# Kernel optimization log

Hardware: AMD Instinct MI355X
Metric: run time of the kernel (lower is better)

The kernel has to match this reference:

```python
import jax, jax.numpy as jnp
import numpy as np

B, P, Q, D_IN, H, DR = 16, 4096, 512, 512, 256, 256


def setup_inputs() -> dict:
    key = jax.random.key(0)
    ks = jax.random.split(key, 6)
    passage = jax.random.normal(ks[0], (B, P, D_IN), dtype=jnp.float32)
    question = jax.random.normal(ks[1], (B, Q, D_IN), dtype=jnp.float32)
    rep = jax.random.normal(ks[2], (B, Q, DR), dtype=jnp.float32)
    rep_p = jax.random.normal(ks[3], (B, P, DR), dtype=jnp.float32)
    p_mask = jnp.zeros((B, P), dtype=bool)  # True = padding position
    q_mask = jnp.zeros((B, Q), dtype=bool)
    # xavier-uniform-like init for U weight, stored as [in, out]
    limit = float(np.sqrt(6.0 / (D_IN + H)))
    W = jax.random.uniform(ks[4], (D_IN, H), dtype=jnp.float32, minval=-limit, maxval=limit)
    D = jnp.ones((1, H), dtype=jnp.float32)
    return {"passage": passage, "p_mask": p_mask, "question": question,
            "q_mask": q_mask, "rep": rep, "rep_p": rep_p, "W": W, "D": D,
            "is_training": 0}


def reference(passage, p_mask, question, q_mask, rep, rep_p, W, D, is_training):
    # inference path (is_training falsy): no dropout
    Up = jax.nn.relu(passage @ W)              # [B, P, H]
    Uq = jax.nn.relu(question @ W) * D         # [B, Q, H], scaled by diagonal D
    scores = jnp.einsum('bph,bqh->bpq', Up, Uq)  # [B, P, Q]
    # question -> passage direction (rep_p is not None)
    scores_T = jnp.where(p_mask[:, None, :], -jnp.inf, scores.transpose(0, 2, 1))  # [B, Q, P]
    alpha_p = jax.nn.softmax(scores_T, axis=-1)
    output_q = jnp.einsum('bqp,bpd->bqd', alpha_p, rep_p)  # [B, Q, DR]
    # passage -> question direction
    scores_m = jnp.where(q_mask[:, None, :], -jnp.inf, scores)  # [B, P, Q]
    alpha = jax.nn.softmax(scores_m, axis=-1)
    output = jnp.einsum('bpq,bqd->bpd', alpha, rep)  # [B, P, DR]
    return (output, output_q)
```

## Files before the change

### kernel.cpp

```cpp
#include <hip/hip_runtime.h>


typedef float  f32x4   __attribute__((ext_vector_type(4)));
typedef float  float4v __attribute__((ext_vector_type(4)));
typedef short  short8v __attribute__((ext_vector_type(8)));
typedef unsigned short us4 __attribute__((ext_vector_type(4)));
typedef unsigned short us8v __attribute__((ext_vector_type(8)));

#define MFMA16(a,b,c) __builtin_amdgcn_mfma_f32_16x16x32_bf16((a),(b),(c),0,0,0)

__device__ __forceinline__ unsigned short f2bf(float f) {
  unsigned int u = __builtin_bit_cast(unsigned int, f);
  u += 0x7FFFu + ((u >> 16) & 1u);
  return (unsigned short)(u >> 16);
}
__device__ __forceinline__ float bf2f(unsigned short h) {
  unsigned int u = (unsigned int)h << 16;
  return __builtin_bit_cast(float, u);
}
__device__ __forceinline__ void split2(float v, unsigned short& h, unsigned short& l) {
  h = f2bf(v);
  l = f2bf(v - bf2f(h));
}
__device__ __forceinline__ unsigned short enc16(float a, float cm) {
  float x = (a - cm + 20.f) * 3276.8f + 0.5f;
  x = fminf(fmaxf(x, 0.f), 65535.f);
  return (unsigned short)x;
}

__device__ __forceinline__ void transpose_body(
    const float* __restrict__ src, unsigned short* __restrict__ dst,
    unsigned short* __restrict__ dstl, int srows, size_t r0, size_t c0,
    int t, float* smemf)
{
#pragma unroll
  for (int j = 0; j < 4; ++j) {
    int idx = j * 256 + t;
    int r = idx >> 4, c4 = (idx & 15) * 4;
    float4v v = *(const float4v*)&src[(r0 + (size_t)r) * 256 + c0 + c4];
    smemf[r * 65 + c4 + 0] = v[0]; smemf[r * 65 + c4 + 1] = v[1];
    smemf[r * 65 + c4 + 2] = v[2]; smemf[r * 65 + c4 + 3] = v[3];
  }
  __syncthreads();
#pragma unroll
  for (int j = 0; j < 4; ++j) {
    int idx = j * 256 + t;
    int dr = idx >> 4, p4 = (idx & 15) * 4;
    size_t o = (c0 + (size_t)dr) * (size_t)srows + r0 + p4;
    if (!dstl) {
      us4 oh;
#pragma unroll
      for (int e = 0; e < 4; ++e) oh[e] = f2bf(smemf[(p4 + e) * 65 + dr]);
      *(us4*)&dst[o] = oh;
    } else {
      us4 oh, ol;
#pragma unroll
      for (int e = 0; e < 4; ++e) {
        unsigned short h, l; split2(smemf[(p4 + e) * 65 + dr], h, l);
        oh[e] = h; ol[e] = l;
      }
      *(us4*)&dst[o] = oh;
      *(us4*)&dstl[o] = ol;
    }
  }
}

template<int APPLY_D>
__device__ __forceinline__ void ugemm_body(
    const float* __restrict__ X,
    const unsigned short* __restrict__ Wth, const unsigned short* __restrict__ Wtl,
    const float* __restrict__ Dv,
    unsigned short* __restrict__ Uh, unsigned short* __restrict__ Ul,
    size_t m0, int t, unsigned char* smem)
{
  unsigned short* lAh = (unsigned short*)smem;
  unsigned short* lAl = (unsigned short*)(smem + 5120);
  unsigned short* lBh = (unsigned short*)(smem + 10240);
  unsigned short* lBl = (unsigned short*)(smem + 30720);
  const int w = t >> 6, l = t & 63;
  const int l15 = l & 15, lg = l >> 4, kr = lg * 8;
  const int arow = t >> 2, ac = (t & 3) * 8;
  const float* asrc = X + (m0 + arow) * 512 + ac;

  f32x4 acc[4][4] = {};
  float4v va0, va1;
  short8v vbh[4], vbl[4];

  va0 = *(const float4v*)(asrc);
  va1 = *(const float4v*)(asrc + 4);
#pragma unroll
  for (int j = 0; j < 4; ++j) {
    int idx = j * 256 + t;
    int row = idx >> 2, c = (idx & 3) * 8;
    size_t g = (size_t)row * 512 + c;
    vbh[j] = *(const short8v*)&Wth[g];
    vbl[j] = *(const short8v*)&Wtl[g];
  }

  for (int k0 = 0; k0 < 512; k0 += 32) {
    short8v ph, pl;
#pragma unroll
    for (int e = 0; e < 4; ++e) {
      unsigned short h, lo;
      split2(va0[e], h, lo); ph[e] = (short)h; pl[e] = (short)lo;
      split2(va1[e], h, lo); ph[4 + e] = (short)h; pl[4 + e] = (short)lo;
    }
    __syncthreads();
    *(short8v*)&lAh[arow * 40 + ac] = ph;
    *(short8v*)&lAl[arow * 40 + ac] = pl;
#pragma unroll
    for (int j = 0; j < 4; ++j) {
      int idx = j * 256 + t;
      int row = idx >> 2, c = (idx & 3) * 8;
      *(short8v*)&lBh[row * 40 + c] = vbh[j];
      *(short8v*)&lBl[row * 40 + c] = vbl[j];
    }
    __syncthreads();
    if (k0 < 480) {
      va0 = *(const float4v*)(asrc + k0 + 32);
      va1 = *(const float4v*)(asrc + k0 + 36);
#pragma unroll
      for (int j = 0; j < 4; ++j) {
        int idx = j * 256 + t;
        int row = idx >> 2, c = (idx & 3) * 8;
        size_t g = (size_t)row * 512 + k0 + 32 + c;
        vbh[j] = *(const short8v*)&Wth[g];
        vbl[j] = *(const short8v*)&Wtl[g];
      }
    }
    short8v ah[4], al[4];
#pragma unroll
    for (int mi = 0; mi < 4; ++mi) {
      ah[mi] = *(const short8v*)&lAh[(mi * 16 + l15) * 40 + kr];
      al[mi] = *(const short8v*)&lAl[(mi * 16 + l15) * 40 + kr];
    }
#pragma unroll
    for (int ni = 0; ni < 4; ++ni) {
      int rr = (w * 64 + ni * 16 + l15) * 40 + kr;
      short8v bh = *(const short8v*)&lBh[rr];
      short8v bl = *(const short8v*)&lBl[rr];
#pragma unroll
      for (int mi = 0; mi < 4; ++mi) {
        acc[mi][ni] = MFMA16(ah[mi], bh, acc[mi][ni]);
        acc[mi][ni] = MFMA16(ah[mi], bl, acc[mi][ni]);
        acc[mi][ni] = MFMA16(al[mi], bh, acc[mi][ni]);
      }
    }
  }
#pragma unroll
  for (int mi = 0; mi < 4; ++mi)
#pragma unroll
    for (int ni = 0; ni < 4; ++ni)
#pragma unroll
      for (int r = 0; r < 4; ++r) {
        size_t row = m0 + mi * 16 + lg * 4 + r;
        int col = w * 64 + ni * 16 + l15;
        float v = acc[mi][ni][r];
        v = v > 0.f ? v : 0.f;
        if (APPLY_D) v *= Dv[col];
        unsigned short h, lo; split2(v, h, lo);
        Uh[row * 256 + col] = h;
        Ul[row * 256 + col] = lo;
      }
}

__global__ __launch_bounds__(256) void transpose_w(
    const float* __restrict__ W,
    unsigned short* __restrict__ Wth, unsigned short* __restrict__ Wtl)
{
  __shared__ float lTf[64 * 65];
  const int blk = blockIdx.x;
  transpose_body(W, Wth, Wtl, 512, (size_t)(blk >> 2) * 64,
                 (size_t)(blk & 3) * 64, threadIdx.x, lTf);
}

__global__ __launch_bounds__(256) void prep_mega(
    const float* __restrict__ passage, const float* __restrict__ question,
    const float* __restrict__ rep, const float* __restrict__ rep_p,
    const unsigned short* __restrict__ Wth, const unsigned short* __restrict__ Wtl,
    const float* __restrict__ Dv,
    unsigned short* __restrict__ Uph, unsigned short* __restrict__ Upl,
    unsigned short* __restrict__ Uqh, unsigned short* __restrict__ Uql,
    unsigned short* __restrict__ repT, unsigned short* __restrict__ repTp)
{
  __shared__ __align__(16) unsigned char smem[51200];
  const int blk = blockIdx.x;
  const int t = threadIdx.x;
  if (blk < 1024) {
    ugemm_body<0>(passage, Wth, Wtl, nullptr, Uph, Upl,
                  (size_t)blk * 64, t, smem);
  } else if (blk < 1152) {
    ugemm_body<1>(question, Wth, Wtl, Dv, Uqh, Uql,
                  (size_t)(blk - 1024) * 64, t, smem);
  } else if (blk < 5248) {
    int rel = blk - 1152;
    int b = rel >> 8, tb = rel & 255;
    transpose_body(rep_p + (size_t)b * 4096 * 256,
                   repTp + (size_t)b * 256 * 4096, nullptr, 4096,
                   (size_t)(tb >> 2) * 64, (size_t)(tb & 3) * 64, t,
                   (float*)smem);
  } else {
    int rel = blk - 5248;
    int b = rel >> 5, tb = rel & 31;
    transpose_body(rep + (size_t)b * 512 * 256,
                   repT + (size_t)b * 256 * 512, nullptr, 512,
                   (size_t)(tb >> 2) * 64, (size_t)(tb & 3) * 64, t,
                   (float*)smem);
  }
}

__global__ __launch_bounds__(256) void transpose_all(
    const float* __restrict__ W, const float* __restrict__ rep,
    const float* __restrict__ rep_p,
    unsigned short* __restrict__ Wth, unsigned short* __restrict__ Wtl,
    unsigned short* __restrict__ repT, unsigned short* __restrict__ repTp)
{
  __shared__ float lTf[64 * 65];
  const int blk = blockIdx.x;
  const int t = threadIdx.x;
  if (blk < 4096) {
    int b = blk >> 8, tb = blk & 255;
    transpose_body(rep_p + (size_t)b * 4096 * 256,
                   repTp + (size_t)b * 256 * 4096, nullptr, 4096,
                   (size_t)(tb >> 2) * 64, (size_t)(tb & 3) * 64, t, lTf);
  } else if (blk < 4608) {
    int rel = blk - 4096; int b = rel >> 5, tb = rel & 31;
    transpose_body(rep + (size_t)b * 512 * 256,
                   repT + (size_t)b * 256 * 512, nullptr, 512,
                   (size_t)(tb >> 2) * 64, (size_t)(tb & 3) * 64, t, lTf);
  } else {
    int rel = blk - 4608;
    transpose_body(W, Wth, Wtl, 512, (size_t)(rel >> 2) * 64,
                   (size_t)(rel & 3) * 64, t, lTf);
  }
}

template<int APPLY_D>
__global__ __launch_bounds__(256) void ugemm_kernel(
    const float* __restrict__ X,
    const unsigned short* __restrict__ Wth, const unsigned short* __restrict__ Wtl,
    const float* __restrict__ Dv,
    unsigned short* __restrict__ Uh, unsigned short* __restrict__ Ul)
{
  __shared__ __align__(16) unsigned char smem[51200];
  ugemm_body<APPLY_D>(X, Wth, Wtl, Dv, Uh, Ul,
                      (size_t)blockIdx.x * 64, threadIdx.x, smem);
}

template<int STORE_S>
__global__ __launch_bounds__(512, 4) void dir2_kernel(
    const unsigned short* __restrict__ Uph, const unsigned short* __restrict__ Upl,
    const unsigned short* __restrict__ Uqh, const unsigned short* __restrict__ Uql,
    const unsigned short* __restrict__ repT, const unsigned char* __restrict__ qmask,
    const unsigned char* __restrict__ pmask, unsigned short* __restrict__ St,
    float* __restrict__ colmaxP, float* __restrict__ out)
{
  __shared__ __align__(16) unsigned char smem[68608];
  unsigned short* probs = (unsigned short*)smem;
  float* smax = (float*)(smem + 66560);
  float* ssum = (float*)(smem + 67584);

  const int id = blockIdx.x;
  const int b  = (id & 7) | ((id >> 9) << 3);
  const int p0 = ((id >> 3) & 63) * 64;
  const int t = threadIdx.x;
  const int w = t >> 6, l = t & 63;
  const int wr = w >> 2, wc = w & 3;
  const int l15 = l & 15, lg = l >> 4, kr = lg * 8;
  const int srow = t >> 2, sc = (t & 3) * 8;

  const unsigned short* UqBh = Uqh + (size_t)b * 512 * 256;
  const unsigned short* UqBl = Uql + (size_t)b * 512 * 256;
  const size_t aoff = ((size_t)b * 4096 + p0 + wr * 32 + l15) * 256 + kr;
  const unsigned short* pAh0 = Uph + aoff;
  const unsigned short* pAh1 = pAh0 + 16 * 256;
  const unsigned short* pAl0 = Upl + aoff;
  const unsigned short* pAl1 = pAl0 + 16 * 256;

  auto lbh = [&](int buf) { return (unsigned short*)(smem + buf * 20480); };
  auto lbl = [&](int buf) { return (unsigned short*)(smem + buf * 20480 + 10240); };

  f32x4 acc[2][8] = {};
  short8v cah0, cah1, cal0, cal1;
  short8v nah0, nah1, nal0, nal1;
  short8v rh, rl;

  cah0 = *(const short8v*)&pAh0[0];
  cah1 = *(const short8v*)&pAh1[0];
  cal0 = *(const short8v*)&pAl0[0];
  cal1 = *(const short8v*)&pAl1[0];
  {
    size_t g = (size_t)srow * 256 + sc;
    rh = *(const short8v*)&UqBh[g];
    rl = *(const short8v*)&UqBl[g];
  }
  *(short8v*)&lbh(0)[srow * 40 + sc] = rh;
  *(short8v*)&lbl(0)[srow * 40 + sc] = rl;
  __syncthreads();

  for (int k0 = 0; k0 < 8; ++k0) {
#pragma unroll
    for (int qh = 0; qh < 4; ++qh) {
      const int cur = qh & 1;
      const bool last = (k0 == 7) && (qh == 3);
      if (!last) {
        int nk0 = (qh == 3) ? k0 + 1 : k0;
        int nqh = (qh == 3) ? 0 : qh + 1;
        size_t g = (size_t)(nqh * 128 + srow) * 256 + nk0 * 32 + sc;
        rh = *(const short8v*)&UqBh[g];
        rl = *(const short8v*)&UqBl[g];
      }
      if (qh == 3 && k0 < 7) {
        size_t ao = (size_t)(k0 + 1) * 32;
        nah0 = *(const short8v*)&pAh0[ao];
        nah1 = *(const short8v*)&pAh1[ao];
        nal0 = *(const short8v*)&pAl0[ao];
        nal1 = *(const short8v*)&pAl1[ao];
      }
      const unsigned short* bhp = lbh(cur);
      const unsigned short* blp = lbl(cur);
#pragma unroll
      for (int qi = 0; qi < 2; ++qi) {
        int rr = (wc * 32 + qi * 16 + l15) * 40 + kr;
        short8v bh = *(const short8v*)&bhp[rr];
        short8v bl = *(const short8v*)&blp[rr];
        int j = qh * 2 + qi;
        acc[0][j] = MFMA16(cah0, bh, acc[0][j]);
        acc[0][j] = MFMA16(cah0, bl, acc[0][j]);
        acc[0][j] = MFMA16(cal0, bh, acc[0][j]);
        acc[1][j] = MFMA16(cah1, bh, acc[1][j]);
        acc[1][j] = MFMA16(cah1, bl, acc[1][j]);
        acc[1][j] = MFMA16(cal1, bh, acc[1][j]);
      }
      if (!last) {
        *(short8v*)&lbh(cur ^ 1)[srow * 40 + sc] = rh;
        *(short8v*)&lbl(cur ^ 1)[srow * 40 + sc] = rl;
      }
      if (qh == 3 && k0 < 7) { cah0 = nah0; cah1 = nah1; cal0 = nal0; cal1 = nal1; }
      __syncthreads();
    }
  }
  if (STORE_S) {
    const unsigned char* pmk = pmask + (size_t)b * 4096 + p0 + wr * 32;
    unsigned int pmw0 = *(const unsigned int*)&pmk[lg * 4];
    unsigned int pmw1 = *(const unsigned int*)&pmk[16 + lg * 4];
#pragma unroll
    for (int j = 0; j < 8; ++j) {
      int qcol = ((j >> 1) << 7) + wc * 32 + ((j & 1) << 4) + l15;
      float a0[4], a1[4];
      float cm = -1e30f;
#pragma unroll
      for (int r = 0; r < 4; ++r) {
        a0[r] = ((pmw0 >> (8 * r)) & 0xFFu) ? -1e30f : acc[0][j][r];
        a1[r] = ((pmw1 >> (8 * r)) & 0xFFu) ? -1e30f : acc[1][j][r];
        cm = fmaxf(cm, fmaxf(a0[r], a1[r]));
      }
      cm = fmaxf(cm, __shfl_xor(cm, 16));
      cm = fmaxf(cm, __shfl_xor(cm, 32));
      us4 e0, e1;
#pragma unroll
      for (int r = 0; r < 4; ++r) {
        e0[r] = enc16(a0[r], cm);
        e1[r] = enc16(a1[r], cm);
      }
      size_t sb = ((size_t)b * 512 + qcol) * 4096 + p0 + wr * 32 + lg * 4;
      *(us4*)&St[sb]      = e0;
      *(us4*)&St[sb + 16] = e1;
      if (l < 16)
        colmaxP[((size_t)b * 128 + (p0 >> 5) + wr) * 512 + qcol] = cm;
    }
  }
  const unsigned char* qm = qmask + (size_t)b * 512;
#pragma unroll
  for (int j = 0; j < 8; ++j) {
    int qcol = ((j >> 1) << 7) + wc * 32 + ((j & 1) << 4) + l15;
    if (qm[qcol]) {
#pragma unroll
      for (int mi = 0; mi < 2; ++mi)
#pragma unroll
        for (int r = 0; r < 4; ++r) acc[mi][j][r] = -1e30f;
    }
  }
#pragma unroll
  for (int mi = 0; mi < 2; ++mi)
#pragma unroll
    for (int r = 0; r < 4; ++r) {
      float v = acc[mi][0][r];
#pragma unroll
      for (int j = 1; j < 8; ++j) v = fmaxf(v, acc[mi][j][r]);
      v = fmaxf(v, __shfl_xor(v, 1)); v = fmaxf(v, __shfl_xor(v, 2));
      v = fmaxf(v, __shfl_xor(v, 4)); v = fmaxf(v, __shfl_xor(v, 8));
      if (l15 == 0) smax[wc * 64 + wr * 32 + mi * 16 + lg * 4 + r] = v;
    }
  __syncthreads();
  float Mx[2][4];
#pragma unroll
  for (int mi = 0; mi < 2; ++mi)
#pragma unroll
    for (int r = 0; r < 4; ++r) {
      int row = wr * 32 + mi * 16 + lg * 4 + r;
      Mx[mi][r] = fmaxf(fmaxf(smax[row], smax[64 + row]),
                        fmaxf(smax[128 + row], smax[192 + row]));
    }
  float rs[2][4] = {};
#pragma unroll
  for (int mi = 0; mi < 2; ++mi)
#pragma unroll
    for (int j = 0; j < 8; ++j)
#pragma unroll
      for (int r = 0; r < 4; ++r) {
        float ev = __expf(acc[mi][j][r] - Mx[mi][r]);
        acc[mi][j][r] = ev;
        rs[mi][r] += ev;
      }
#pragma unroll
  for (int mi = 0; mi < 2; ++mi)
#pragma unroll
    for (int r = 0; r < 4; ++r) {
      float v = rs[mi][r];
      v += __shfl_xor(v, 1); v += __shfl_xor(v, 2);
      v += __shfl_xor(v, 4); v += __shfl_xor(v, 8);
      if (l15 == 0) ssum[wc * 64 + wr * 32 + mi * 16 + lg * 4 + r] = v;
    }
#pragma unroll
  for (int mi = 0; mi < 2; ++mi)
#pragma unroll
    for (int j = 0; j < 8; ++j) {
      int qcol = ((j >> 1) << 7) + wc * 32 + ((j & 1) << 4) + l15;
#pragma unroll
      for (int r = 0; r < 4; ++r)
        probs[(wr * 32 + mi * 16 + lg * 4 + r) * 520 + qcol] = f2bf(acc[mi][j][r]);
    }
  __syncthreads();
  const unsigned short* rT = repT + (size_t)b * 131072;
  float invv[4][4];
#pragma unroll
  for (int mi = 0; mi < 4; ++mi)
#pragma unroll
    for (int r = 0; r < 4; ++r) {
      int row = mi * 16 + lg * 4 + r;
      invv[mi][r] = 1.0f / (ssum[row] + ssum[64 + row] +
                            ssum[128 + row] + ssum[192 + row]);
    }
  f32x4 acc2[4][2] = {};
  const unsigned short* rTb = rT + (size_t)(w * 32 + l15) * 512 + kr;
  short8v cb0 = *(const short8v*)(rTb);
  short8v cb1 = *(const short8v*)(rTb + 16 * 512);
  for (int k0 = 0; k0 < 512; k0 += 32) {
    int kn = (k0 + 32) & 511;
    short8v nb0 = *(const short8v*)(rTb + kn);
    short8v nb1 = *(const short8v*)(rTb + 16 * 512 + kn);
    short8v a0 = *(const short8v*)&probs[(l15) * 520 + k0 + kr];
    short8v a1 = *(const short8v*)&probs[(16 + l15) * 520 + k0 + kr];
    short8v a2 = *(const short8v*)&probs[(32 + l15) * 520 + k0 + kr];
    short8v a3 = *(const short8v*)&probs[(48 + l15) * 520 + k0 + kr];
    acc2[0][0] = MFMA16(a0, cb0, acc2[0][0]);
    acc2[1][0] = MFMA16(a1, cb0, acc2[1][0]);
    acc2[2][0] = MFMA16(a2, cb0, acc2[2][0]);
    acc2[3][0] = MFMA16(a3, cb0, acc2[3][0]);
    acc2[0][1] = MFMA16(a0, cb1, acc2[0][1]);
    acc2[1][1] = MFMA16(a1, cb1, acc2[1][1]);
    acc2[2][1] = MFMA16(a2, cb1, acc2[2][1]);
    acc2[3][1] = MFMA16(a3, cb1, acc2[3][1]);
    cb0 = nb0; cb1 = nb1;
  }
#pragma unroll
  for (int mi = 0; mi < 4; ++mi)
#pragma unroll
    for (int di = 0; di < 2; ++di)
#pragma unroll
      for (int r = 0; r < 4; ++r) {
        int row = p0 + mi * 16 + lg * 4 + r;
        int col = w * 32 + di * 16 + l15;
        out[((size_t)b * 4096 + row) * 256 + col] = acc2[mi][di][r] * invv[mi][r];
      }
}

__global__ __launch_bounds__(256) void dir1_pv(
    const unsigned short* __restrict__ St, const float* __restrict__ colmaxP,
    const unsigned short* __restrict__ repTp,
    float* __restrict__ accP, float* __restrict__ mlP)
{
  __shared__ unsigned short lAe[2][32 * 72];
  const int id = blockIdx.x;
  const int xcd = id & 7, r0 = id >> 3;
  const int b = xcd * 2 + (r0 >> 6);
  const int rem = r0 & 63;
  const int qt = rem >> 2, ch = rem & 3;
  const int q0 = qt * 32, pbeg = ch * 1024;
  const int pi = (b * 16 + qt) * 4 + ch;
  const int NT = 16;

  const int t = threadIdx.x;
  const int w = t >> 6, l = t & 63;
  const int l15 = l & 15, lg = l >> 4, kr = lg * 8;
  const int srow = t >> 3, sp = (t & 7) * 8;

  const float* cmq = colmaxP + (size_t)b * 128 * 512 + q0 + srow;
  float mq_s;
  {
    const int part = t & 7;
    float m = -1e30f;
#pragma unroll
    for (int j = 0; j < 16; ++j)
      m = fmaxf(m, cmq[(size_t)(part + j * 8) * 512]);
    m = fmaxf(m, __shfl_xor(m, 1));
    m = fmaxf(m, __shfl_xor(m, 2));
    m = fmaxf(m, __shfl_xor(m, 4));
    mq_s = m;
  }
  const unsigned short* Sb = St + ((size_t)b * 512 + q0 + srow) * 4096;
  const unsigned short* vtb = repTp + ((size_t)b * 256 + w * 64 + l15) * 4096;
  float rsum = 0.f;
  f32x4 acc[2][4] = {};
  us8v u; float cmv;
  short8v bvA[2][4], bvB[2][4];

  auto STAGE_LOAD = [&](int tile) {
    int pelem = pbeg + tile * 64 + sp;
    u = *(const us8v*)(Sb + pelem);
    cmv = cmq[(size_t)(pelem >> 5) * 512];
  };
  auto STAGE_FINISH = [&](int buf) {
    float base = cmv - 20.f - mq_s;
    short8v pk;
#pragma unroll
    for (int e = 0; e < 8; ++e) {
      float ev = __expf((float)u[e] * (1.f / 3276.8f) + base);
      rsum += ev;
      pk[e] = (short)f2bf(ev);
    }
    *(short8v*)&lAe[buf][srow * 72 + sp] = pk;
  };
  auto BV_LOAD = [&](int tile, short8v (&bv)[2][4]) {
    int p0v = pbeg + tile * 64;
#pragma unroll
    for (int ks = 0; ks < 2; ++ks)
#pragma unroll
      for (int di = 0; di < 4; ++di)
        bv[ks][di] = *(const short8v*)&vtb[(size_t)(di * 16) * 4096 + p0v + ks * 32 + kr];
  };
  auto COMPUTE = [&](int buf, short8v (&bv)[2][4]) {
#pragma unroll
    for (int ks = 0; ks < 2; ++ks) {
      short8v pa0 = *(const short8v*)&lAe[buf][l15 * 72 + ks * 32 + kr];
      short8v pa1 = *(const short8v*)&lAe[buf][(16 + l15) * 72 + ks * 32 + kr];
#pragma unroll
      for (int di = 0; di < 4; ++di) {
        acc[0][di] = MFMA16(pa0, bv[ks][di], acc[0][di]);
        acc[1][di] = MFMA16(pa1, bv[ks][di], acc[1][di]);
      }
    }
  };

  STAGE_LOAD(0);
  BV_LOAD(0, bvA);
  STAGE_FINISH(0);
  STAGE_LOAD(1);
  __syncthreads();

#pragma unroll 1
  for (int tt = 0; tt < NT; tt += 2) {
    const bool has1 = (tt + 1 < NT), has2 = (tt + 2 < NT), has3 = (tt + 3 < NT);
    if (has1) BV_LOAD(tt + 1, bvB);
    COMPUTE(0, bvA);
    if (has1) STAGE_FINISH(1);
    if (has2) STAGE_LOAD(tt + 2);
    __syncthreads();
    if (has1) {
      if (has2) BV_LOAD(tt + 2, bvA);
      COMPUTE(1, bvB);
      if (has2) STAGE_FINISH(0);
      if (has3) STAGE_LOAD(tt + 3);
      __syncthreads();
    }
  }

  rsum += __shfl_xor(rsum, 1);
  rsum += __shfl_xor(rsum, 2);
  rsum += __shfl_xor(rsum, 4);
  if ((t & 7) == 0) mlP[(size_t)pi * 32 + srow] = rsum;

  float* ab = accP + (size_t)pi * 32 * 256;
#pragma unroll
  for (int mi = 0; mi < 2; ++mi)
#pragma unroll
    for (int di = 0; di < 4; ++di)
#pragma unroll
      for (int r = 0; r < 4; ++r) {
        int row = mi * 16 + lg * 4 + r;
        int col = w * 64 + di * 16 + l15;
        ab[(size_t)row * 256 + col] = acc[mi][di][r];
      }
}

__global__ __launch_bounds__(256) void merge4_kernel(
    const float* __restrict__ accP, const float* __restrict__ mlP,
    float* __restrict__ outq)
{
  const int g = blockIdx.x * 256 + threadIdx.x;
  const int row = g >> 6;
  const int d0 = (g & 63) * 4;
  const int b = row >> 9, q = row & 511;
  const int qt = q >> 5, ri = q & 31;
  const int pbase = (b * 16 + qt) * 4;
  float s = 0.f;
  float4v o = {0.f, 0.f, 0.f, 0.f};
#pragma unroll
  for (int c = 0; c < 4; ++c) {
    s += mlP[(size_t)(pbase + c) * 32 + ri];
    float4v a = *(const float4v*)&accP[((size_t)(pbase + c) * 32 + ri) * 256 + d0];
#pragma unroll
    for (int k = 0; k < 4; ++k) o[k] += a[k];
  }
  float inv = 1.0f / s;
#pragma unroll
  for (int k = 0; k < 4; ++k) o[k] *= inv;
  *(float4v*)&outq[(size_t)row * 256 + d0] = o;
}

__global__ __launch_bounds__(256) void dir1_partial(
    const unsigned short* __restrict__ Uph, const unsigned short* __restrict__ Upl,
    const unsigned short* __restrict__ Uqh, const unsigned short* __restrict__ Uql,
    const unsigned short* __restrict__ repTp, const unsigned char* __restrict__ pmask,
    float* __restrict__ accP, float* __restrict__ mlP)
{
  __shared__ __align__(16) unsigned char smem[39424];
  unsigned short* lAh = (unsigned short*)smem;
  unsigned short* lAl = (unsigned short*)(smem + 16896);
  unsigned short* lP  = (unsigned short*)(smem + 33792);
  float* smax = (float*)(smem + 38400);
  float* ssum = (float*)(smem + 38912);

  const int id  = blockIdx.x;
  const int xcd = id & 7, rr0 = id >> 3;
  const int b   = xcd * 2 + (rr0 >> 6);
  const int rem = rr0 & 63;
  const int qt  = rem >> 2, ch = rem & 3;
  const int q0  = qt * 32;
  const int pbeg = ch * 1024;
  const int pi  = (b * 16 + qt) * 4 + ch;

  const int t = threadIdx.x;
  const int w = t >> 6, l = t & 63;
  const int l15 = l & 15, lg = l >> 4, kr = lg * 8;

#pragma unroll
  for (int j = 0; j < 4; ++j) {
    int idx = j * 256 + t;
    int row = idx >> 5, c = (idx & 31) * 8;
    size_t g = ((size_t)b * 512 + q0 + row) * 256 + c;
    *(short8v*)&lAh[row * 264 + c] = *(const short8v*)&Uqh[g];
    *(short8v*)&lAl[row * 264 + c] = *(const short8v*)&Uql[g];
  }
  float m_r[2][4], l_r[2][4];
#pragma unroll
  for (int mi = 0; mi < 2; ++mi)
#pragma unroll
    for (int r = 0; r < 4; ++r) { m_r[mi][r] = -1e30f; l_r[mi][r] = 0.f; }
  f32x4 accO[2][4] = {};
  const size_t upoff = ((size_t)b * 4096 + w * 16 + l15) * 256;
  const unsigned short* upbh = Uph + upoff;
  const unsigned short* upbl = Upl + upoff;
  const unsigned short* vtb = repTp + (size_t)b * 1048576;
  const unsigned char* pm = pmask + (size_t)b * 4096;
  __syncthreads();

  for (int p0 = pbeg; p0 < pbeg + 1024; p0 += 64) {
    f32x4 s[2] = {};
#pragma unroll
    for (int k0 = 0; k0 < 256; k0 += 32) {
      short8v ah0 = *(const short8v*)&lAh[l15 * 264 + k0 + kr];
      short8v ah1 = *(const short8v*)&lAh[(16 + l15) * 264 + k0 + kr];
      short8v al0 = *(const short8v*)&lAl[l15 * 264 + k0 + kr];
      short8v al1 = *(const short8v*)&lAl[(16 + l15) * 264 + k0 + kr];
      short8v bvh = *(const short8v*)&upbh[(size_t)p0 * 256 + k0 + kr];
      short8v bvl = *(const short8v*)&upbl[(size_t)p0 * 256 + k0 + kr];
      s[0] = MFMA16(ah0, bvh, s[0]);
      s[0] = MFMA16(ah0, bvl, s[0]);
      s[0] = MFMA16(al0, bvh, s[0]);
      s[1] = MFMA16(ah1, bvh, s[1]);
      s[1] = MFMA16(ah1, bvl, s[1]);
      s[1] = MFMA16(al1, bvh, s[1]);
    }
    if (pm[p0 + w * 16 + l15]) {
#pragma unroll
      for (int mi = 0; mi < 2; ++mi)
#pragma unroll
        for (int r = 0; r < 4; ++r) s[mi][r] = -1e30f;
    }
#pragma unroll
    for (int mi = 0; mi < 2; ++mi)
#pragma unroll
      for (int r = 0; r < 4; ++r) {
        float v = s[mi][r];
        v = fmaxf(v, __shfl_xor(v, 1)); v = fmaxf(v, __shfl_xor(v, 2));
        v = fmaxf(v, __shfl_xor(v, 4)); v = fmaxf(v, __shfl_xor(v, 8));
        if (l15 == 0) smax[w * 32 + mi * 16 + lg * 4 + r] = v;
      }
    __syncthreads();
    float mnew[2][4], fsc[2][4], e[2][4];
#pragma unroll
    for (int mi = 0; mi < 2; ++mi)
#pragma unroll
      for (int r = 0; r < 4; ++r) {
        int row = mi * 16 + lg * 4 + r;
        float tm = fmaxf(fmaxf(smax[row], smax[32 + row]),
                         fmaxf(smax[64 + row], smax[96 + row]));
        float mn = fmaxf(m_r[mi][r], tm);
        mnew[mi][r] = mn;
        fsc[mi][r] = __expf(m_r[mi][r] - mn);
        e[mi][r] = __expf(s[mi][r] - mn);
      }
#pragma unroll
    for (int mi = 0; mi < 2; ++mi)
#pragma unroll
      for (int r = 0; r < 4; ++r) {
        float v = e[mi][r];
        v += __shfl_xor(v, 1); v += __shfl_xor(v, 2);
        v += __shfl_xor(v, 4); v += __shfl_xor(v, 8);
        if (l15 == 0) ssum[w * 32 + mi * 16 + lg * 4 + r] = v;
        lP[(mi * 16 + lg * 4 + r) * 72 + w * 16 + l15] = f2bf(e[mi][r]);
      }
    __syncthreads();
#pragma unroll
    for (int mi = 0; mi < 2; ++mi)
#pragma unroll
      for (int r = 0; r < 4; ++r) {
        int row = mi * 16 + lg * 4 + r;
        float ts = ssum[row] + ssum[32 + row] + ssum[64 + row] + ssum[96 + row];
        l_r[mi][r] = l_r[mi][r] * fsc[mi][r] + ts;
        m_r[mi][r] = mnew[mi][r];
      }
#pragma unroll
    for (int mi = 0; mi < 2; ++mi)
#pragma unroll
      for (int di = 0; di < 4; ++di)
#pragma unroll
        for (int r = 0; r < 4; ++r) accO[mi][di][r] *= fsc[mi][r];
#pragma unroll
    for (int ks = 0; ks < 64; ks += 32) {
      short8v pa0 = *(const short8v*)&lP[l15 * 72 + ks + kr];
      short8v pa1 = *(const short8v*)&lP[(16 + l15) * 72 + ks + kr];
#pragma unroll
      for (int di = 0; di < 4; ++di) {
        short8v bv = *(const short8v*)&vtb[(size_t)(w * 64 + di * 16 + l15) * 4096 + p0 + ks + kr];
        accO[0][di] = MFMA16(pa0, bv, accO[0][di]);
        accO[1][di] = MFMA16(pa1, bv, accO[1][di]);
      }
    }
  }
  float* ab = accP + (size_t)pi * 32 * 256;
#pragma unroll
  for (int mi = 0; mi < 2; ++mi)
#pragma unroll
    for (int di = 0; di < 4; ++di)
#pragma unroll
      for (int r = 0; r < 4; ++r) {
        int row = mi * 16 + lg * 4 + r;
        int col = w * 64 + di * 16 + l15;
        ab[(size_t)row * 256 + col] = accO[mi][di][r];
      }
  if (w == 0 && l15 == 0) {
#pragma unroll
    for (int mi = 0; mi < 2; ++mi)
#pragma unroll
      for (int r = 0; r < 4; ++r) {
        int row = mi * 16 + lg * 4 + r;
        mlP[((size_t)pi * 32 + row) * 2 + 0] = m_r[mi][r];
        mlP[((size_t)pi * 32 + row) * 2 + 1] = l_r[mi][r];
      }
  }
}

__global__ __launch_bounds__(256) void merge_kernel(
    const float* __restrict__ accP, const float* __restrict__ mlP,
    float* __restrict__ outq)
{
  const int g = blockIdx.x * 256 + threadIdx.x;
  const int row = g >> 6;
  const int d0 = (g & 63) * 4;
  const int b = row >> 9, q = row & 511;
  const int qt = q >> 5, ri = q & 31;
  const int pbase = (b * 16 + qt) * 4;
  float m[4], lv[4];
  float M = -1e30f;
#pragma unroll
  for (int c = 0; c < 4; ++c) {
    m[c]  = mlP[((size_t)(pbase + c) * 32 + ri) * 2 + 0];
    lv[c] = mlP[((size_t)(pbase + c) * 32 + ri) * 2 + 1];
    M = fmaxf(M, m[c]);
  }
  float s = 0.f;
  float4v o = {0.f, 0.f, 0.f, 0.f};
#pragma unroll
  for (int c = 0; c < 4; ++c) {
    float e = __expf(m[c] - M);
    s += e * lv[c];
    float4v a = *(const float4v*)&accP[((size_t)(pbase + c) * 32 + ri) * 256 + d0];
#pragma unroll
    for (int k = 0; k < 4; ++k) o[k] += e * a[k];
  }
  float inv = 1.0f / s;
#pragma unroll
  for (int k = 0; k < 4; ++k) o[k] *= inv;
  *(float4v*)&outq[(size_t)row * 256 + d0] = o;
}

extern "C" void kernel_launch(void* const* d_in, const int* in_sizes, int n_in,
                              void* d_out, int out_size, void* d_ws, size_t ws_size,
                              hipStream_t stream) {
  (void)in_sizes; (void)n_in; (void)out_size;
  const float* passage        = (const float*)d_in[0];
  const unsigned char* p_mask = (const unsigned char*)d_in[1];
  const float* question       = (const float*)d_in[2];
  const unsigned char* q_mask = (const unsigned char*)d_in[3];
  const float* rep            = (const float*)d_in[4];
  const float* rep_p          = (const float*)d_in[5];
  const float* W              = (const float*)d_in[6];
  const float* Dv             = (const float*)d_in[7];

  unsigned short* Wth   = (unsigned short*)d_ws;
  unsigned short* Wtl   = Wth   + 131072;
  unsigned short* repT  = Wtl   + 131072;
  unsigned short* repTp = repT  + 2097152;
  unsigned short* Uqh   = repTp + 16777216;
  unsigned short* Uql   = Uqh   + 2097152;
  unsigned short* Uph   = Uql   + 2097152;
  unsigned short* Upl   = Uph   + 16777216;
  unsigned short* StU = (unsigned short*)((char*)d_ws + 113770496ULL);
  float* colmaxP      = (float*)((char*)d_ws + 180879360ULL);
  const size_t NEEDED = 185073664ULL;

  float* out  = (float*)d_out;
  float* outq = out + (size_t)16 * 4096 * 256;

  if (ws_size >= NEEDED) {
    float* accP4 = (float*)Uph;
    float* mlP4  = (float*)Uqh;
    transpose_w<<<32, 256, 0, stream>>>(W, Wth, Wtl);
    prep_mega<<<5760, 256, 0, stream>>>(passage, question, rep, rep_p,
                                        Wth, Wtl, Dv, Uph, Upl, Uqh, Uql,
                                        repT, repTp);
    dir2_kernel<1><<<1024, 512, 0, stream>>>(Uph, Upl, Uqh, Uql, repT,
                                             q_mask, p_mask, StU, colmaxP, out);
    dir1_pv<<<1024, 256, 0, stream>>>(StU, colmaxP, repTp, accP4, mlP4);
    merge4_kernel<<<2048, 256, 0, stream>>>(accP4, mlP4, outq);
  } else {
    float* accP = out;
    float* mlP  = (float*)Wth;
    transpose_all<<<4640, 256, 0, stream>>>(W, rep, rep_p, Wth, Wtl, repT, repTp);
    ugemm_kernel<0><<<1024, 256, 0, stream>>>(passage,  Wth, Wtl, nullptr, Uph, Upl);
    ugemm_kernel<1><<<128,  256, 0, stream>>>(question, Wth, Wtl, Dv,      Uqh, Uql);
    dir1_partial<<<1024, 256, 0, stream>>>(Uph, Upl, Uqh, Uql, repTp, p_mask, accP, mlP);
    merge_kernel<<<2048, 256, 0, stream>>>(accP, mlP, outq);
    dir2_kernel<0><<<1024, 512, 0, stream>>>(Uph, Upl, Uqh, Uql, repT,
                                             q_mask, nullptr, nullptr, nullptr, out);
  }
}
```

Baseline: 312.2 us.

## Double dir2 P-tile to 128 rows with 1024-thread blocks and split PV stage

Each dir2 block now covers 128 passage rows with 16 waves instead of 64 rows with 8 waves. The staged Uq tiles in shared memory are therefore reused across twice as many rows, and only half the threads load them. Because the probability buffer still holds 64 rows, the softmax-times-rep stage runs in two halves, with each wave producing 16 output columns. The cost is that repT is re-read per half, there are fewer MFMAs per B load, and the block count halves. The register cap from launch bounds of 1024 threads with 4 blocks may also cause spills.

```diff
diff --git a/kernel.cpp b/kernel.cpp
--- a/kernel.cpp
+++ b/kernel.cpp
@@ -248,26 +248,27 @@
 }
 
 template<int STORE_S>
-__global__ __launch_bounds__(512, 4) void dir2_kernel(
+__global__ __launch_bounds__(1024, 4) void dir2_kernel(
     const unsigned short* __restrict__ Uph, const unsigned short* __restrict__ Upl,
     const unsigned short* __restrict__ Uqh, const unsigned short* __restrict__ Uql,
     const unsigned short* __restrict__ repT, const unsigned char* __restrict__ qmask,
     const unsigned char* __restrict__ pmask, unsigned short* __restrict__ St,
     float* __restrict__ colmaxP, float* __restrict__ out)
 {
-  __shared__ __align__(16) unsigned char smem[68608];
+  __shared__ __align__(16) unsigned char smem[70656];
   unsigned short* probs = (unsigned short*)smem;
   float* smax = (float*)(smem + 66560);
-  float* ssum = (float*)(smem + 67584);
+  float* ssum = (float*)(smem + 68608);
 
   const int id = blockIdx.x;
-  const int b  = (id & 7) | ((id >> 9) << 3);
-  const int p0 = ((id >> 3) & 63) * 64;
+  const int xcd = id & 7, r0b = id >> 3;
+  const int b = xcd * 2 + (r0b >> 5);
+  const int p0 = (r0b & 31) * 128;
   const int t = threadIdx.x;
   const int w = t >> 6, l = t & 63;
   const int wr = w >> 2, wc = w & 3;
   const int l15 = l & 15, lg = l >> 4, kr = lg * 8;
-  const int srow = t >> 2, sc = (t & 3) * 8;
+  const int srow = (t >> 2) & 127, sc = (t & 3) * 8;
 
   const unsigned short* UqBh = Uqh + (size_t)b * 512 * 256;
   const unsigned short* UqBl = Uql + (size_t)b * 512 * 256;
@@ -289,13 +290,13 @@
   cah1 = *(const short8v*)&pAh1[0];
   cal0 = *(const short8v*)&pAl0[0];
   cal1 = *(const short8v*)&pAl1[0];
-  {
+  if (t < 512) {
     size_t g = (size_t)srow * 256 + sc;
     rh = *(const short8v*)&UqBh[g];
     rl = *(const short8v*)&UqBl[g];
-  }
-  *(short8v*)&lbh(0)[srow * 40 + sc] = rh;
-  *(short8v*)&lbl(0)[srow * 40 + sc] = rl;
+    *(short8v*)&lbh(0)[srow * 40 + sc] = rh;
+    *(short8v*)&lbl(0)[srow * 40 + sc] = rl;
+  }
   __syncthreads();
 
   for (int k0 = 0; k0 < 8; ++k0) {
@@ -303,7 +304,7 @@
     for (int qh = 0; qh < 4; ++qh) {
       const int cur = qh & 1;
       const bool last = (k0 == 7) && (qh == 3);
-      if (!last) {
+      if (!last && t < 512) {
         int nk0 = (qh == 3) ? k0 + 1 : k0;
         int nqh = (qh == 3) ? 0 : qh + 1;
         size_t g = (size_t)(nqh * 128 + srow) * 256 + nk0 * 32 + sc;
@@ -332,7 +333,7 @@
         acc[1][j] = MFMA16(cah1, bl, acc[1][j]);
         acc[1][j] = MFMA16(cal1, bh, acc[1][j]);
       }
-      if (!last) {
+      if (!last && t < 512) {
         *(short8v*)&lbh(cur ^ 1)[srow * 40 + sc] = rh;
         *(short8v*)&lbl(cur ^ 1)[srow * 40 + sc] = rl;
       }
@@ -390,7 +391,7 @@
       for (int j = 1; j < 8; ++j) v = fmaxf(v, acc[mi][j][r]);
       v = fmaxf(v, __shfl_xor(v, 1)); v = fmaxf(v, __shfl_xor(v, 2));
       v = fmaxf(v, __shfl_xor(v, 4)); v = fmaxf(v, __shfl_xor(v, 8));
-      if (l15 == 0) smax[wc * 64 + wr * 32 + mi * 16 + lg * 4 + r] = v;
+      if (l15 == 0) smax[wc * 128 + wr * 32 + mi * 16 + lg * 4 + r] = v;
     }
   __syncthreads();
   float Mx[2][4];
@@ -399,8 +400,8 @@
 #pragma unroll
     for (int r = 0; r < 4; ++r) {
       int row = wr * 32 + mi * 16 + lg * 4 + r;
-      Mx[mi][r] = fmaxf(fmaxf(smax[row], smax[64 + row]),
-                        fmaxf(smax[128 + row], smax[192 + row]));
+      Mx[mi][r] = fmaxf(fmaxf(smax[row], smax[128 + row]),
+                        fmaxf(smax[256 + row], smax[384 + row]));
     }
   float rs[2][4] = {};
 #pragma unroll
@@ -420,60 +421,59 @@
       float v = rs[mi][r];
       v += __shfl_xor(v, 1); v += __shfl_xor(v, 2);
       v += __shfl_xor(v, 4); v += __shfl_xor(v, 8);
-      if (l15 == 0) ssum[wc * 64 + wr * 32 + mi * 16 + lg * 4 + r] = v;
-    }
-#pragma unroll
-  for (int mi = 0; mi < 2; ++mi)
-#pragma unroll
-    for (int j = 0; j < 8; ++j) {
-      int qcol = ((j >> 1) << 7) + wc * 32 + ((j & 1) << 4) + l15;
-#pragma unroll
-      for (int r = 0; r < 4; ++r)
-        probs[(wr * 32 + mi * 16 + lg * 4 + r) * 520 + qcol] = f2bf(acc[mi][j][r]);
-    }
-  __syncthreads();
+      if (l15 == 0) ssum[wc * 128 + wr * 32 + mi * 16 + lg * 4 + r] = v;
+    }
   const unsigned short* rT = repT + (size_t)b * 131072;
-  float invv[4][4];
-#pragma unroll
-  for (int mi = 0; mi < 4; ++mi)
-#pragma unroll
-    for (int r = 0; r < 4; ++r) {
-      int row = mi * 16 + lg * 4 + r;
-      invv[mi][r] = 1.0f / (ssum[row] + ssum[64 + row] +
-                            ssum[128 + row] + ssum[192 + row]);
-    }
-  f32x4 acc2[4][2] = {};
-  const unsigned short* rTb = rT + (size_t)(w * 32 + l15) * 512 + kr;
-  short8v cb0 = *(const short8v*)(rTb);
-  short8v cb1 = *(const short8v*)(rTb + 16 * 512);
-  for (int k0 = 0; k0 < 512; k0 += 32) {
-    int kn = (k0 + 32) & 511;
-    short8v nb0 = *(const short8v*)(rTb + kn);
-    short8v nb1 = *(const short8v*)(rTb + 16 * 512 + kn);
-    short8v a0 = *(const short8v*)&probs[(l15) * 520 + k0 + kr];
-    short8v a1 = *(const short8v*)&probs[(16 + l15) * 520 + k0 + kr];
-    short8v a2 = *(const short8v*)&probs[(32 + l15) * 520 + k0 + kr];
-    short8v a3 = *(const short8v*)&probs[(48 + l15) * 520 + k0 + kr];
-    acc2[0][0] = MFMA16(a0, cb0, acc2[0][0]);
-    acc2[1][0] = MFMA16(a1, cb0, acc2[1][0]);
-    acc2[2][0] = MFMA16(a2, cb0, acc2[2][0]);
-    acc2[3][0] = MFMA16(a3, cb0, acc2[3][0]);
-    acc2[0][1] = MFMA16(a0, cb1, acc2[0][1]);
-    acc2[1][1] = MFMA16(a1, cb1, acc2[1][1]);
-    acc2[2][1] = MFMA16(a2, cb1, acc2[2][1]);
-    acc2[3][1] = MFMA16(a3, cb1, acc2[3][1]);
-    cb0 = nb0; cb1 = nb1;
-  }
-#pragma unroll
-  for (int mi = 0; mi < 4; ++mi)
-#pragma unroll
-    for (int di = 0; di < 2; ++di)
-#pragma unroll
-      for (int r = 0; r < 4; ++r) {
-        int row = p0 + mi * 16 + lg * 4 + r;
-        int col = w * 32 + di * 16 + l15;
-        out[((size_t)b * 4096 + row) * 256 + col] = acc2[mi][di][r] * invv[mi][r];
-      }
+  const unsigned short* rTb = rT + (size_t)(w * 16 + l15) * 512 + kr;
+#pragma unroll
+  for (int h = 0; h < 2; ++h) {
+    __syncthreads();
+    if ((wr >> 1) == h) {
+      const int lr0 = (wr & 1) * 32;
+#pragma unroll
+      for (int mi = 0; mi < 2; ++mi)
+#pragma unroll
+        for (int j = 0; j < 8; ++j) {
+          int qcol = ((j >> 1) << 7) + wc * 32 + ((j & 1) << 4) + l15;
+#pragma unroll
+          for (int r = 0; r < 4; ++r)
+            probs[(lr0 + mi * 16 + lg * 4 + r) * 520 + qcol] = f2bf(acc[mi][j][r]);
+        }
+    }
+    __syncthreads();
+    float invv[4][4];
+#pragma unroll
+    for (int mi = 0; mi < 4; ++mi)
+#pragma unroll
+      for (int r = 0; r < 4; ++r) {
+        int row = h * 64 + mi * 16 + lg * 4 + r;
+        invv[mi][r] = 1.0f / (ssum[row] + ssum[128 + row] +
+                              ssum[256 + row] + ssum[384 + row]);
+      }
+    f32x4 acc2[4] = {};
+    short8v cb = *(const short8v*)(rTb);
+    for (int k0 = 0; k0 < 512; k0 += 32) {
+      int kn = (k0 + 32) & 511;
+      short8v nb = *(const short8v*)(rTb + kn);
+      short8v a0 = *(const short8v*)&probs[(l15) * 520 + k0 + kr];
+      short8v a1 = *(const short8v*)&probs[(16 + l15) * 520 + k0 + kr];
+      short8v a2 = *(const short8v*)&probs[(32 + l15) * 520 + k0 + kr];
+      short8v a3 = *(const short8v*)&probs[(48 + l15) * 520 + k0 + kr];
+      acc2[0] = MFMA16(a0, cb, acc2[0]);
+      acc2[1] = MFMA16(a1, cb, acc2[1]);
+      acc2[2] = MFMA16(a2, cb, acc2[2]);
+      acc2[3] = MFMA16(a3, cb, acc2[3]);
+      cb = nb;
+    }
+#pragma unroll
+    for (int mi = 0; mi < 4; ++mi)
+#pragma unroll
+      for (int r = 0; r < 4; ++r) {
+        int row = p0 + h * 64 + mi * 16 + lg * 4 + r;
+        int col = w * 16 + l15;
+        out[((size_t)b * 4096 + row) * 256 + col] = acc2[mi][r] * invv[mi][r];
+      }
+  }
 }
 
 __global__ __launch_bounds__(256) void dir1_pv(
@@ -842,7 +842,7 @@
     prep_mega<<<5760, 256, 0, stream>>>(passage, question, rep, rep_p,
                                         Wth, Wtl, Dv, Uph, Upl, Uqh, Uql,
                                         repT, repTp);
-    dir2_kernel<1><<<1024, 512, 0, stream>>>(Uph, Upl, Uqh, Uql, repT,
+    dir2_kernel<1><<<512, 1024, 0, stream>>>(Uph, Upl, Uqh, Uql, repT,
                                              q_mask, p_mask, StU, colmaxP, out);
     dir1_pv<<<1024, 256, 0, stream>>>(StU, colmaxP, repTp, accP4, mlP4);
     merge4_kernel<<<2048, 256, 0, stream>>>(accP4, mlP4, outq);
@@ -854,7 +854,7 @@
     ugemm_kernel<1><<<128,  256, 0, stream>>>(question, Wth, Wtl, Dv,      Uqh, Uql);
     dir1_partial<<<1024, 256, 0, stream>>>(Uph, Upl, Uqh, Uql, repTp, p_mask, accP, mlP);
     merge_kernel<<<2048, 256, 0, stream>>>(accP, mlP, outq);
-    dir2_kernel<0><<<1024, 512, 0, stream>>>(Uph, Upl, Uqh, Uql, repT,
+    dir2_kernel<0><<<512, 1024, 0, stream>>>(Uph, Upl, Uqh, Uql, repT,
                                              q_mask, nullptr, nullptr, nullptr, out);
   }
 }
```

Result: no change. 317.6 us (+1.7%).
